# Kernel optimization log

Hardware: AMD Instinct MI355X
Metric: run time of the kernel (lower is better)

## Reference

```python
import jax, jax.numpy as jnp
import numpy as np

B = 8192
IN = 2048
H = 2048


def setup_inputs() -> dict:
    key = jax.random.key(0)
    ks = jax.random.split(key, 6)
    stdv = 1.0 / np.sqrt(H)
    return {
        "x": jax.random.normal(ks[0], (B, IN), dtype=jnp.float32),
        "h_prev": jax.random.normal(ks[1], (B, H), dtype=jnp.float32),
        "c_prev": jax.random.normal(ks[2], (B, H), dtype=jnp.float32),
        "weight_ih": jax.random.normal(ks[3], (4 * H, IN), dtype=jnp.float32) * stdv,
        "weight_hh": jax.random.normal(ks[4], (4 * H, H), dtype=jnp.float32) * stdv,
        "bias": jax.random.normal(ks[5], (4 * H,), dtype=jnp.float32) * stdv,
    }


def reference(x, h_prev, c_prev, weight_ih, weight_hh, bias):
    # gates: [B, 4H] = x @ W_ih^T + h_prev @ W_hh^T + b
    gates = x @ weight_ih.T + h_prev @ weight_hh.T + bias
    i, f, j, o = jnp.split(gates, 4, axis=1)
    i = jax.nn.sigmoid(i)
    f = jax.nn.sigmoid(f)
    o = jax.nn.sigmoid(o)
    j = jnp.tanh(j)
    # cap_input_gate=True: input gate capped by (1 - f)
    c = f * c_prev + jnp.minimum(1.0 - f, i) * j
    h = o * jnp.tanh(c)
    return (h, c)
```

## Files before the change

kernel.cpp:

```cpp
#include <hip/hip_runtime.h>

#define DEVI __device__ __forceinline__

typedef __attribute__((ext_vector_type(8))) __bf16 bf16x8;
typedef __attribute__((ext_vector_type(4))) float floatx4;

constexpr int Bsz = 8192;
constexpr int Hd  = 2048;
constexpr int INd = 2048;
constexpr int N1  = Bsz * INd;

DEVI unsigned short f2bf_rne(float f) {
  unsigned int u = __float_as_uint(f);
  u += 0x7FFFu + ((u >> 16) & 1u);
  return (unsigned short)(u >> 16);
}

__global__ void cvt4(const float* __restrict__ s0, const float* __restrict__ s1,
                     const float* __restrict__ s2, const float* __restrict__ s3,
                     unsigned short* __restrict__ dst) {
  const float* src = (blockIdx.y == 0) ? s0 : (blockIdx.y == 1) ? s1
                   : (blockIdx.y == 2) ? s2 : s3;
  unsigned short* out = dst + (size_t)blockIdx.y * N1;
  const int nv = N1 / 4;
  for (int i = blockIdx.x * blockDim.x + threadIdx.x; i < nv;
       i += gridDim.x * blockDim.x) {
    float4 v = ((const float4*)src)[i];
    ushort4 o;
    o.x = f2bf_rne(v.x); o.y = f2bf_rne(v.y);
    o.z = f2bf_rne(v.z); o.w = f2bf_rne(v.w);
    ((ushort4*)out)[i] = o;
  }
}

DEVI void gload_lds16(const void* g, void* l) {
  __builtin_amdgcn_global_load_lds(
      (const __attribute__((address_space(1))) void*)g,
      (__attribute__((address_space(3))) void*)l, 16, 0, 0);
}

DEVI float sigm(float x) { return 1.0f / (1.0f + __expf(-x)); }
DEVI float tanh_fast(float x) { return 1.0f - 2.0f / (1.0f + __expf(2.0f * x)); }

__global__ __launch_bounds__(512, 4) void lstm_gemm(
    const unsigned short* __restrict__ ws,
    const float* __restrict__ bias,
    const float* __restrict__ c_prev,
    float* __restrict__ out_h,
    float* __restrict__ out_c) {
  __shared__ __align__(16) unsigned short sm[2 * (256 + 128) * 32];
  char* smc = (char*)sm;

  const unsigned short* xb  = ws;
  const unsigned short* hb  = ws + (size_t)N1;
  const unsigned short* wih = ws + (size_t)2 * N1;
  const unsigned short* whh = ws + (size_t)3 * N1;

  const int tid  = threadIdx.x;
  const int lane = tid & 63;
  const int wid  = tid >> 6;
  const int wm   = wid >> 1;
  const int wn   = wid & 1;
  const int lr   = lane & 15, lk = lane >> 4;

  const int wg = blockIdx.x;
  const int x8 = wg & 7;
  const int lc = wg >> 3;
  const int bc = (x8 & 3) * 16 + (lc & 15);
  const int rb = ((x8 >> 2) * 16 + (lc >> 4)) * 256;

  unsigned int aOff[2], bOff;
#pragma unroll
  for (int j = 0; j < 2; ++j) {
    const int r = wid * 32 + j * 16 + (lane >> 2);
    aOff[j] = (unsigned)(rb + r) * 2048u + (unsigned)((lane & 3) * 8);
  }
  {
    const int r = wid * 16 + (lane >> 2);
    const int gate = (r >> 4) & 3, wnn = r >> 6;
    const int wrow = gate * 2048 + bc * 32 + wnn * 16 + (r & 15);
    bOff = (unsigned)wrow * 2048u + (unsigned)((lane & 3) * 8);
  }

  const char* pA = smc + wm * 4096 + lr * 64 + lk * 16;
  const char* pB = smc + 32768 + wn * 4096 + lr * 64 + lk * 16;

  floatx4 acc[4][4];
#pragma unroll
  for (int a = 0; a < 4; ++a)
#pragma unroll
    for (int b = 0; b < 4; ++b)
      acc[a][b] = (floatx4){0.f, 0.f, 0.f, 0.f};

#define STAGE_A(ts) {                                                         \
    const int p_ = (ts) & 1;                                                  \
    const unsigned short* s_ = (((ts) < 64) ? xb : hb) + (((ts) & 63) * 32);  \
    gload_lds16(s_ + aOff[0], smc + p_ * 16384 + wid * 2048);                 \
    gload_lds16(s_ + aOff[1], smc + p_ * 16384 + wid * 2048 + 1024); }
#define STAGE_B(ts) {                                                         \
    const int p_ = (ts) & 1;                                                  \
    const unsigned short* s_ = (((ts) < 64) ? wih : whh) + (((ts) & 63) * 32);\
    gload_lds16(s_ + bOff, smc + 32768 + p_ * 8192 + wid * 1024); }

#define LDA2(D, P, QM)                                                        \
  _Pragma("unroll") for (int m = 0; m < 2; ++m)                               \
    D[m] = *(const bf16x8*)(pA + ((P) * 16384 + ((QM) * 2 + m) * 1024));
#define LDB2(D, P, QN)                                                        \
  _Pragma("unroll") for (int n = 0; n < 2; ++n)                               \
    D[n] = *(const bf16x8*)(pB + ((P) * 8192 + ((QN) * 2 + n) * 1024));
#define MM4(AF, BF, QM, QN)                                                   \
  __builtin_amdgcn_s_setprio(1);                                              \
  _Pragma("unroll") for (int m = 0; m < 2; ++m)                               \
    _Pragma("unroll") for (int n = 0; n < 2; ++n)                             \
      acc[(QM) * 2 + m][(QN) * 2 + n] =                                       \
          __builtin_amdgcn_mfma_f32_16x16x32_bf16(                            \
              AF[m], BF[n], acc[(QM) * 2 + m][(QN) * 2 + n], 0, 0, 0);        \
  __builtin_amdgcn_s_setprio(0);
#define BAR  asm volatile("s_barrier" ::: "memory")
#define VM2  asm volatile("s_waitcnt vmcnt(2)" ::: "memory")
#define VM0  asm volatile("s_waitcnt vmcnt(0)" ::: "memory")
#define NOP  (void)0

#define KTILE(P, S1, S3, W) {                                                 \
    bf16x8 a0[2], a1[2], b0[2], b1[2];                                        \
    LDA2(a0, P, 0); LDB2(b0, P, 0); S1;                                       \
    MM4(a0, b0, 0, 0);                                                        \
    LDA2(a1, P, 1);                                                           \
    MM4(a1, b0, 1, 0); BAR;                                                   \
    LDB2(b1, P, 1); S3;                                                       \
    MM4(a1, b1, 1, 1);                                                        \
    MM4(a0, b1, 0, 1); W; BAR;                                                \
  }

  STAGE_A(0); STAGE_B(0); STAGE_A(1);
  VM0;
  BAR;

  for (int u = 0; u < 63; ++u) {
    const int t0 = 2 * u;
    KTILE(0, STAGE_B(t0 + 1), STAGE_A(t0 + 2), VM2);
    KTILE(1, STAGE_B(t0 + 2), STAGE_A(t0 + 3), VM2);
  }
  KTILE(0, STAGE_B(127), NOP, VM0);
  KTILE(1, NOP, NOP, NOP);

  const int hcol = bc * 32 + wn * 16 + lr;
  const float b_i = bias[hcol];
  const float b_f = bias[2048 + hcol];
  const float b_j = bias[4096 + hcol];
  const float b_o = bias[6144 + hcol];
#pragma unroll
  for (int mf = 0; mf < 4; ++mf)
#pragma unroll
    for (int r = 0; r < 4; ++r) {
      const int row = rb + wm * 64 + mf * 16 + lk * 4 + r;
      const float gi = acc[mf][0][r] + b_i;
      const float gf = acc[mf][1][r] + b_f;
      const float gj = acc[mf][2][r] + b_j;
      const float go = acc[mf][3][r] + b_o;
      const float iv = sigm(gi);
      const float fv = sigm(gf);
      const float jv = tanh_fast(gj);
      const float ov = sigm(go);
      const size_t idx = (size_t)row * 2048 + hcol;
      const float cp = c_prev[idx];
      const float cv = fv * cp + fminf(1.0f - fv, iv) * jv;
      out_h[idx] = ov * tanh_fast(cv);
      out_c[idx] = cv;
    }
}

extern "C" void kernel_launch(void* const* d_in, const int* in_sizes, int n_in,
                              void* d_out, int out_size, void* d_ws, size_t ws_size,
                              hipStream_t stream) {
  const float* x      = (const float*)d_in[0];
  const float* h_prev = (const float*)d_in[1];
  const float* c_prev = (const float*)d_in[2];
  const float* w_ih   = (const float*)d_in[3];
  const float* w_hh   = (const float*)d_in[4];
  const float* bias   = (const float*)d_in[5];

  float* out_h = (float*)d_out;
  float* out_c = out_h + (size_t)Bsz * Hd;
  unsigned short* wsb = (unsigned short*)d_ws;

  dim3 cgrid(2048, 4);
  cvt4<<<cgrid, 256, 0, stream>>>(x, h_prev, w_ih, w_hh, wsb);

  lstm_gemm<<<2048, 512, 0, stream>>>(wsb, bias, c_prev, out_h, out_c);
}
```

Measured before the change: 618.9 us.

## Enlarge LSTM GEMM block tile to 256x256 with K=64 and swizzled LDS

Each workgroup now computes a 256-row by 64-hidden-column (256 gate columns) tile with 16 waves, and stages K=64 slices instead of 32. This halves the number of workgroups and K iterations, aiming to raise operand reuse per global and LDS load. An XOR swizzle is applied to the global-to-LDS layout and the fragment reads to avoid LDS bank conflicts on the wider rows. In exchange the kernel needs 128KB of LDS per block, which allows only one block per CU. The launch bounds ask for 1024 threads with 4 blocks, which may force a tight register budget.

Result: faster. 517.3 us (-16.4%).

```diff
diff --git a/kernel.cpp b/kernel.cpp
--- a/kernel.cpp
+++ b/kernel.cpp
@@ -42,13 +42,13 @@
 DEVI float sigm(float x) { return 1.0f / (1.0f + __expf(-x)); }
 DEVI float tanh_fast(float x) { return 1.0f - 2.0f / (1.0f + __expf(2.0f * x)); }
 
-__global__ __launch_bounds__(512, 4) void lstm_gemm(
+__global__ __launch_bounds__(1024, 4) void lstm_gemm(
     const unsigned short* __restrict__ ws,
     const float* __restrict__ bias,
     const float* __restrict__ c_prev,
     float* __restrict__ out_h,
     float* __restrict__ out_c) {
-  __shared__ __align__(16) unsigned short sm[2 * (256 + 128) * 32];
+  __shared__ __align__(16) unsigned short sm[4 * 256 * 64];
   char* smc = (char*)sm;
 
   const unsigned short* xb  = ws;
@@ -59,31 +59,35 @@
   const int tid  = threadIdx.x;
   const int lane = tid & 63;
   const int wid  = tid >> 6;
-  const int wm   = wid >> 1;
-  const int wn   = wid & 1;
+  const int wm   = wid >> 2;
+  const int wn   = wid & 3;
   const int lr   = lane & 15, lk = lane >> 4;
+  const int lr8  = lane >> 3;
+  const int swc  = ((lane & 7) ^ lr8) * 8;
 
   const int wg = blockIdx.x;
   const int x8 = wg & 7;
   const int lc = wg >> 3;
-  const int bc = (x8 & 3) * 16 + (lc & 15);
-  const int rb = ((x8 >> 2) * 16 + (lc >> 4)) * 256;
+  const int bc = (x8 & 3) * 8 + (lc & 7);
+  const int rb = ((x8 >> 2) * 16 + (lc >> 3)) * 256;
 
-  unsigned int aOff[2], bOff;
+  unsigned int aOff[2], bOff[2];
 #pragma unroll
   for (int j = 0; j < 2; ++j) {
-    const int r = wid * 32 + j * 16 + (lane >> 2);
-    aOff[j] = (unsigned)(rb + r) * 2048u + (unsigned)((lane & 3) * 8);
-  }
-  {
-    const int r = wid * 16 + (lane >> 2);
-    const int gate = (r >> 4) & 3, wnn = r >> 6;
-    const int wrow = gate * 2048 + bc * 32 + wnn * 16 + (r & 15);
-    bOff = (unsigned)wrow * 2048u + (unsigned)((lane & 3) * 8);
+    const int r = wid * 16 + j * 8 + lr8;
+    aOff[j] = (unsigned)(rb + r) * 2048u + (unsigned)swc;
+    const int wrow = ((r >> 4) & 3) * 2048 + bc * 64 + (r >> 6) * 16 + (r & 15);
+    bOff[j] = (unsigned)wrow * 2048u + (unsigned)swc;
   }
 
-  const char* pA = smc + wm * 4096 + lr * 64 + lk * 16;
-  const char* pB = smc + 32768 + wn * 4096 + lr * 64 + lk * 16;
+  const char* pA[2];
+  const char* pB[2];
+#pragma unroll
+  for (int s = 0; s < 2; ++s) {
+    const int phys = (s * 4 + lk) ^ (lr & 7);
+    pA[s] = smc + wm * 8192 + lr * 128 + phys * 16;
+    pB[s] = smc + 65536 + wn * 8192 + lr * 128 + phys * 16;
+  }
 
   floatx4 acc[4][4];
 #pragma unroll
@@ -94,27 +98,31 @@
 
 #define STAGE_A(ts) {                                                         \
     const int p_ = (ts) & 1;                                                  \
-    const unsigned short* s_ = (((ts) < 64) ? xb : hb) + (((ts) & 63) * 32);  \
-    gload_lds16(s_ + aOff[0], smc + p_ * 16384 + wid * 2048);                 \
-    gload_lds16(s_ + aOff[1], smc + p_ * 16384 + wid * 2048 + 1024); }
+    const unsigned short* s_ = (((ts) < 32) ? xb : hb) + (((ts) & 31) * 64);  \
+    gload_lds16(s_ + aOff[0], smc + p_ * 32768 + wid * 2048);                 \
+    gload_lds16(s_ + aOff[1], smc + p_ * 32768 + wid * 2048 + 1024); }
 #define STAGE_B(ts) {                                                         \
     const int p_ = (ts) & 1;                                                  \
-    const unsigned short* s_ = (((ts) < 64) ? wih : whh) + (((ts) & 63) * 32);\
-    gload_lds16(s_ + bOff, smc + 32768 + p_ * 8192 + wid * 1024); }
+    const unsigned short* s_ = (((ts) < 32) ? wih : whh) + (((ts) & 31) * 64);\
+    gload_lds16(s_ + bOff[0], smc + 65536 + p_ * 32768 + wid * 2048);         \
+    gload_lds16(s_ + bOff[1], smc + 65536 + p_ * 32768 + wid * 2048 + 1024); }
 
-#define LDA2(D, P, QM)                                                        \
+#define LDA2(D, P, QH)                                                        \
   _Pragma("unroll") for (int m = 0; m < 2; ++m)                               \
-    D[m] = *(const bf16x8*)(pA + ((P) * 16384 + ((QM) * 2 + m) * 1024));
-#define LDB2(D, P, QN)                                                        \
+    _Pragma("unroll") for (int s = 0; s < 2; ++s)                             \
+      D[m][s] = *(const bf16x8*)(pA[s] + ((P) * 32768 + ((QH) * 2 + m) * 2048));
+#define LDB2(D, P, QH)                                                        \
   _Pragma("unroll") for (int n = 0; n < 2; ++n)                               \
-    D[n] = *(const bf16x8*)(pB + ((P) * 8192 + ((QN) * 2 + n) * 1024));
-#define MM4(AF, BF, QM, QN)                                                   \
+    _Pragma("unroll") for (int s = 0; s < 2; ++s)                             \
+      D[n][s] = *(const bf16x8*)(pB[s] + ((P) * 32768 + ((QH) * 2 + n) * 2048));
+#define MFMA8(AF, BF, QM, QN)                                                 \
   __builtin_amdgcn_s_setprio(1);                                              \
   _Pragma("unroll") for (int m = 0; m < 2; ++m)                               \
     _Pragma("unroll") for (int n = 0; n < 2; ++n)                             \
-      acc[(QM) * 2 + m][(QN) * 2 + n] =                                       \
-          __builtin_amdgcn_mfma_f32_16x16x32_bf16(                            \
-              AF[m], BF[n], acc[(QM) * 2 + m][(QN) * 2 + n], 0, 0, 0);        \
+      _Pragma("unroll") for (int s = 0; s < 2; ++s)                           \
+        acc[(QM) * 2 + m][(QN) * 2 + n] =                                     \
+            __builtin_amdgcn_mfma_f32_16x16x32_bf16(                          \
+                AF[m][s], BF[n][s], acc[(QM) * 2 + m][(QN) * 2 + n], 0, 0, 0);\
   __builtin_amdgcn_s_setprio(0);
 #define BAR  asm volatile("s_barrier" ::: "memory")
 #define VM2  asm volatile("s_waitcnt vmcnt(2)" ::: "memory")
@@ -122,29 +130,29 @@
 #define NOP  (void)0
 
 #define KTILE(P, S1, S3, W) {                                                 \
-    bf16x8 a0[2], a1[2], b0[2], b1[2];                                        \
-    LDA2(a0, P, 0); LDB2(b0, P, 0); S1;                                       \
-    MM4(a0, b0, 0, 0);                                                        \
-    LDA2(a1, P, 1);                                                           \
-    MM4(a1, b0, 1, 0); BAR;                                                   \
-    LDB2(b1, P, 1); S3;                                                       \
-    MM4(a1, b1, 1, 1);                                                        \
-    MM4(a0, b1, 0, 1); W; BAR;                                                \
+    bf16x8 a01[2][2], a23[2][2], b01[2][2], b23[2][2];                        \
+    LDA2(a01, P, 0); LDB2(b01, P, 0); S1;                                     \
+    MFMA8(a01, b01, 0, 0);                                                    \
+    LDA2(a23, P, 1);                                                          \
+    MFMA8(a23, b01, 1, 0); BAR;                                               \
+    LDB2(b23, P, 1); S3;                                                      \
+    MFMA8(a23, b23, 1, 1);                                                    \
+    MFMA8(a01, b23, 0, 1); W; BAR;                                            \
   }
 
   STAGE_A(0); STAGE_B(0); STAGE_A(1);
   VM0;
   BAR;
 
-  for (int u = 0; u < 63; ++u) {
+  for (int u = 0; u < 31; ++u) {
     const int t0 = 2 * u;
     KTILE(0, STAGE_B(t0 + 1), STAGE_A(t0 + 2), VM2);
     KTILE(1, STAGE_B(t0 + 2), STAGE_A(t0 + 3), VM2);
   }
-  KTILE(0, STAGE_B(127), NOP, VM0);
+  KTILE(0, STAGE_B(63), NOP, VM0);
   KTILE(1, NOP, NOP, NOP);
 
-  const int hcol = bc * 32 + wn * 16 + lr;
+  const int hcol = bc * 64 + wn * 16 + lr;
   const float b_i = bias[hcol];
   const float b_f = bias[2048 + hcol];
   const float b_j = bias[4096 + hcol];
@@ -187,5 +195,5 @@
   dim3 cgrid(2048, 4);
   cvt4<<<cgrid, 256, 0, stream>>>(x, h_prev, w_ih, w_hh, wsb);
 
-  lstm_gemm<<<2048, 512, 0, stream>>>(wsb, bias, c_prev, out_h, out_c);
+  lstm_gemm<<<1024, 1024, 0, stream>>>(wsb, bias, c_prev, out_h, out_c);
 }
```
